# Performance work log

Measured on AMD Instinct MI355X. Metric: run time of the kernel, lower is better.

The kernel has to match this reference:

```python
import jax, jax.numpy as jnp
import numpy as np

HEADS = 4
TOKEN_DIM = 128
SCALE = (TOKEN_DIM // HEADS) ** -0.5


def _conv1x1(x, w, b):
    # x: (B,C,D,H,W), w: (O,C), b: (O,)
    return jnp.einsum('bcdhw,oc->bodhw', x, w) + b[None, :, None, None, None]


def _flatten(x):
    # (B,C,D,H,W) -> (B,L,C)
    B, C = x.shape[0], x.shape[1]
    return x.reshape(B, C, -1).transpose(0, 2, 1)


def _mha(q, k, v):
    # q: (B,Lq,D), k/v: (B,Lk,D)
    B, Lq, Dq = q.shape
    Lk = k.shape[1]
    hd = Dq // HEADS
    qh = q.reshape(B, Lq, HEADS, hd).transpose(0, 2, 1, 3)
    kh = k.reshape(B, Lk, HEADS, hd).transpose(0, 2, 1, 3)
    vh = v.reshape(B, Lk, HEADS, hd).transpose(0, 2, 1, 3)
    attn = jnp.einsum('bhqd,bhkd->bhqk', qh, kh) * SCALE
    attn = jax.nn.softmax(attn, axis=-1)
    out = jnp.einsum('bhqk,bhkd->bhqd', attn, vh)
    return out.transpose(0, 2, 1, 3).reshape(B, Lq, Dq)


def setup_inputs() -> dict:
    key = jax.random.key(0)
    ks = jax.random.split(key, 10)
    B, C, D, H, W = 2, 64, 16, 16, 16
    return {
        'feat_ct': jax.random.normal(ks[0], (B, C, D, H, W), jnp.float32),
        'feat_pet': jax.random.normal(ks[1], (B, C, D, H, W), jnp.float32),
        'wq': jax.random.normal(ks[2], (TOKEN_DIM, C), jnp.float32) * 0.05,
        'bq': jax.random.normal(ks[3], (TOKEN_DIM,), jnp.float32) * 0.05,
        'wk': jax.random.normal(ks[4], (TOKEN_DIM, C), jnp.float32) * 0.05,
        'bk': jax.random.normal(ks[5], (TOKEN_DIM,), jnp.float32) * 0.05,
        'wv': jax.random.normal(ks[6], (TOKEN_DIM, C), jnp.float32) * 0.05,
        'bv': jax.random.normal(ks[7], (TOKEN_DIM,), jnp.float32) * 0.05,
        'wo': jax.random.normal(ks[8], (C, TOKEN_DIM), jnp.float32) * 0.05,
        'bo': jax.random.normal(ks[9], (C,), jnp.float32) * 0.05,
    }


def reference(feat_ct, feat_pet, wq, bq, wk, bk, wv, bv, wo, bo):
    B, C, D, H, W = feat_ct.shape
    q_ct = _flatten(_conv1x1(feat_ct, wq, bq))
    k_ct = _flatten(_conv1x1(feat_ct, wk, bk))
    v_ct = _flatten(_conv1x1(feat_ct, wv, bv))
    q_pet = _flatten(_conv1x1(feat_pet, wq, bq))
    k_pet = _flatten(_conv1x1(feat_pet, wk, bk))
    v_pet = _flatten(_conv1x1(feat_pet, wv, bv))

    ct_attn = _mha(q_ct, k_pet, v_pet)
    pet_attn = _mha(q_pet, k_ct, v_ct)

    # Original torch code does view(B, token_dim, -1).permute(0,2,1) followed by
    # unflatten's permute(0,2,1) -> net effect is a raw reinterpretation of the
    # contiguous (B, L, token_dim) buffer as (B, token_dim, D, H, W): a reshape.
    fused_ct = ((ct_attn + q_ct) * 0.5).reshape(B, TOKEN_DIM, D, H, W)
    fused_ct = _conv1x1(fused_ct, wo, bo)  # dropout is identity (eval)
    fused_pet = ((pet_attn + q_pet) * 0.5).reshape(B, TOKEN_DIM, D, H, W)
    fused_pet = _conv1x1(fused_pet, wo, bo)

    return feat_ct + fused_ct, feat_pet + fused_pet
```

## Files before the change

### kernel.cpp

```cpp
#include <hip/hip_runtime.h>

typedef __bf16 bf16x8 __attribute__((ext_vector_type(8)));
typedef float f32x4 __attribute__((ext_vector_type(4)));
typedef float f32x16 __attribute__((ext_vector_type(16)));
typedef _Float16 f16x2 __attribute__((ext_vector_type(2)));
typedef unsigned short u16x8 __attribute__((ext_vector_type(8)));
typedef unsigned int u32x4 __attribute__((ext_vector_type(4)));
typedef unsigned int u32x2 __attribute__((ext_vector_type(2)));

constexpr int C_ = 64, TD_ = 128, L_ = 4096, B_ = 2, H_ = 4, HD_ = 32;
constexpr float SCALE_LOG2E = 0.25504821365f;

#if __has_builtin(__builtin_amdgcn_exp2f)
#define EXP2F __builtin_amdgcn_exp2f
#else
#define EXP2F exp2f
#endif

static __device__ __forceinline__ unsigned short f2bf(float f) {
  unsigned u = __builtin_bit_cast(unsigned, f);
  u += 0x7fffu + ((u >> 16) & 1u);
  return (unsigned short)(u >> 16);
}
static __device__ __forceinline__ float bf2f(unsigned short h) {
  unsigned u = ((unsigned)h) << 16;
  return __builtin_bit_cast(float, u);
}
static __device__ __forceinline__ unsigned cvt_pk_bf16(float lo, float hi) {
  unsigned r;
  asm("v_cvt_pk_bf16_f32 %0, %1, %2" : "=v"(r) : "v"(lo), "v"(hi));
  return r;
}
static __device__ __forceinline__ unsigned cvt_pk_f16(float lo, float hi) {
  return __builtin_bit_cast(unsigned, __builtin_amdgcn_cvt_pkrtz(lo, hi));
}
static __device__ __forceinline__ void plane_swap(unsigned& a, unsigned& b) {
  asm("v_permlane32_swap_b32 %0, %1" : "+v"(a), "+v"(b));
}
static __device__ __forceinline__ float xhalf_add(float x) {
  float a = x, b = x;
  asm("v_permlane32_swap_b32 %0, %1" : "+v"(a), "+v"(b));
  return a + b;
}
static __device__ __forceinline__ int rowf(int r, int hi) {
  return (r & 3) + 8 * (r >> 2) + 4 * hi;
}
static __device__ __forceinline__ bf16x8 pack8(const float* v) {
  unsigned p0 = cvt_pk_bf16(v[0], v[1]);
  unsigned p1 = cvt_pk_bf16(v[2], v[3]);
  unsigned p2 = cvt_pk_bf16(v[4], v[5]);
  unsigned p3 = cvt_pk_bf16(v[6], v[7]);
  return __builtin_bit_cast(bf16x8, (u32x4){p0, p1, p2, p3});
}

__global__ __launch_bounds__(256) void proj_kernel(
    const float* __restrict__ fct, const float* __restrict__ fpet,
    const float* __restrict__ wq, const float* __restrict__ bq,
    const float* __restrict__ wk, const float* __restrict__ bk,
    const float* __restrict__ wv, const float* __restrict__ bv,
    unsigned short* __restrict__ Qbf, unsigned short* __restrict__ Kbf,
    unsigned short* __restrict__ Vt, float* __restrict__ QT)
{
  __shared__ __align__(16) unsigned short Tb[32][136];

  int bid = blockIdx.x;
  int lt = bid & 127;
  int rest = bid >> 7;
  int mb = rest & 3;
  int which = rest >> 2;
  int l0 = lt * 32;
  int b = mb & 1;
  const float* xb = (mb >= 2 ? fpet : fct) + (size_t)b * C_ * L_;

  int lane = threadIdx.x & 63, wid = threadIdx.x >> 6;
  int l31 = lane & 31, hi = lane >> 5;
  int od = wid * 32;

  const float* W  = which == 0 ? wq : (which == 1 ? wk : wv);
  const float* Bs = which == 0 ? bq : (which == 1 ? bk : bv);

  const f32x16 Z = {0.f, 0.f, 0.f, 0.f, 0.f, 0.f, 0.f, 0.f,
                    0.f, 0.f, 0.f, 0.f, 0.f, 0.f, 0.f, 0.f};
  f32x16 acc = Z;
  #pragma unroll
  for (int ch = 0; ch < 4; ++ch) {
    float v[8], a[8];
    #pragma unroll
    for (int j = 0; j < 8; ++j)
      v[j] = xb[(size_t)(ch * 16 + hi * 8 + j) * L_ + l0 + l31];
    const float* wr = W + (size_t)(od + l31) * C_ + ch * 16 + hi * 8;
    #pragma unroll
    for (int j = 0; j < 8; ++j) a[j] = wr[j];
    acc = __builtin_amdgcn_mfma_f32_32x32x16_bf16(pack8(a), pack8(v), acc, 0, 0, 0);
  }

  if (which == 2) {
    #pragma unroll
    for (int r = 0; r < 16; ++r) {
      int o = od + rowf(r, hi);
      Vt[((size_t)mb * TD_ + o) * L_ + l0 + l31] = f2bf(acc[r] + Bs[o]);
    }
  } else {
    if (which == 0) {
      #pragma unroll
      for (int r = 0; r < 16; ++r) {
        int o = od + rowf(r, hi);
        QT[((size_t)mb * TD_ + o) * L_ + l0 + l31] = acc[r] + Bs[o];
      }
    }
    float sc = which == 0 ? SCALE_LOG2E : 1.0f;
    #pragma unroll
    for (int rg = 0; rg < 4; ++rg) {
      int cb = od + 8 * rg + 4 * hi;
      float y0 = (acc[rg * 4 + 0] + Bs[cb + 0]) * sc;
      float y1 = (acc[rg * 4 + 1] + Bs[cb + 1]) * sc;
      float y2 = (acc[rg * 4 + 2] + Bs[cb + 2]) * sc;
      float y3 = (acc[rg * 4 + 3] + Bs[cb + 3]) * sc;
      u32x2 pk = {cvt_pk_bf16(y0, y1), cvt_pk_bf16(y2, y3)};
      *(u32x2*)&Tb[l31][cb] = pk;
    }
    __syncthreads();
    unsigned short* dstg = which ? Kbf : Qbf;
    int row = threadIdx.x >> 3, chunk = threadIdx.x & 7;
    int h = chunk >> 1, d0 = (chunk & 1) * 16;
    u16x8 v0 = *(const u16x8*)&Tb[row][chunk * 16];
    u16x8 v1 = *(const u16x8*)&Tb[row][chunk * 16 + 8];
    size_t gb = (((size_t)mb * H_ + h) * L_ + l0 + row) * HD_ + d0;
    *(u16x8*)&dstg[gb] = v0;
    *(u16x8*)&dstg[gb + 8] = v1;
  }
}

static __device__ __forceinline__ void softmax_pv(
    const f32x16& S, float& lp, f32x16& O, bf16x8 vc0, bf16x8 vc1)
{
  float p[16];
  #pragma unroll
  for (int i = 0; i < 16; ++i) p[i] = EXP2F(S[i]);
  float s0 = (p[0] + p[1]) + (p[2] + p[3]);
  float s1 = (p[4] + p[5]) + (p[6] + p[7]);
  float s2 = (p[8] + p[9]) + (p[10] + p[11]);
  float s3 = (p[12] + p[13]) + (p[14] + p[15]);
  lp += (s0 + s1) + (s2 + s3);

  unsigned w0 = cvt_pk_bf16(p[0], p[1]);
  unsigned w1 = cvt_pk_bf16(p[2], p[3]);
  unsigned w2 = cvt_pk_bf16(p[4], p[5]);
  unsigned w3 = cvt_pk_bf16(p[6], p[7]);
  unsigned w4 = cvt_pk_bf16(p[8], p[9]);
  unsigned w5 = cvt_pk_bf16(p[10], p[11]);
  unsigned w6 = cvt_pk_bf16(p[12], p[13]);
  unsigned w7 = cvt_pk_bf16(p[14], p[15]);
  plane_swap(w0, w2);
  plane_swap(w1, w3);
  plane_swap(w4, w6);
  plane_swap(w5, w7);
  bf16x8 pf0 = __builtin_bit_cast(bf16x8, (u32x4){w0, w1, w2, w3});
  bf16x8 pf1 = __builtin_bit_cast(bf16x8, (u32x4){w4, w5, w6, w7});

  O = __builtin_amdgcn_mfma_f32_32x32x16_bf16(vc0, pf0, O, 0, 0, 0);
  O = __builtin_amdgcn_mfma_f32_32x32x16_bf16(vc1, pf1, O, 0, 0, 0);
}

__global__ __launch_bounds__(256, 4) void attn_kernel(
    const unsigned short* __restrict__ Qbf, const unsigned short* __restrict__ Kbf,
    const unsigned short* __restrict__ Vt, const float* __restrict__ QT,
    unsigned short* __restrict__ Fh, unsigned short* __restrict__ Fl)
{
  __shared__ __align__(16) unsigned Obuf[4][64][17];
  __shared__ float lbuf[4][64];

  int bid = blockIdx.x;
  int x = bid & 7, local = bid >> 3;
  int g = 2 * x + (local & 1);
  int qg = local >> 1;
  int h = g & 3, b = (g >> 2) & 1, dir = g >> 3;

  int lane = threadIdx.x & 63, wid = threadIdx.x >> 6;
  int l31 = lane & 31, hi = lane >> 5;
  int q0 = qg * 64;
  int qmb = dir * B_ + b, kmb = (1 - dir) * B_ + b;
  int k0 = wid * 1024;

  const unsigned short* qbase = Qbf + (size_t)(qmb * H_ + h) * L_ * HD_;
  bf16x8 qb[2][2];
  #pragma unroll
  for (int s = 0; s < 2; ++s)
    #pragma unroll
    for (int c = 0; c < 2; ++c)
      qb[s][c] = *(const bf16x8*)(qbase + (q0 + s * 32 + l31) * HD_ + c * 16 + hi * 8);

  const unsigned short* kp =
      Kbf + (size_t)(kmb * H_ + h) * L_ * HD_ + (k0 + l31) * HD_ + hi * 8;
  const unsigned short* vp =
      Vt + (size_t)(kmb * TD_ + h * HD_ + l31) * L_ + k0 + hi * 8;

  const f32x16 Z = {0.f, 0.f, 0.f, 0.f, 0.f, 0.f, 0.f, 0.f,
                    0.f, 0.f, 0.f, 0.f, 0.f, 0.f, 0.f, 0.f};
  f32x16 Oa[2] = {Z, Z};
  float lp[2] = {0.f, 0.f};

  bf16x8 kc0 = *(const bf16x8*)(kp);
  bf16x8 kc1 = *(const bf16x8*)(kp + 16);
  bf16x8 vc0 = *(const bf16x8*)(vp);
  bf16x8 vc1 = *(const bf16x8*)(vp + 16);

  #pragma unroll 4
  for (int t = 0; t < 32; ++t) {
    bf16x8 kn0 = *(const bf16x8*)(kp + (t + 1) * 1024);
    bf16x8 kn1 = *(const bf16x8*)(kp + (t + 1) * 1024 + 16);
    bf16x8 vn0 = *(const bf16x8*)(vp + (t + 1) * 32);
    bf16x8 vn1 = *(const bf16x8*)(vp + (t + 1) * 32 + 16);
    #pragma unroll
    for (int s = 0; s < 2; ++s) {
      f32x16 S = __builtin_amdgcn_mfma_f32_32x32x16_bf16(kc0, qb[s][0], Z, 0, 0, 0);
      S = __builtin_amdgcn_mfma_f32_32x32x16_bf16(kc1, qb[s][1], S, 0, 0, 0);
      softmax_pv(S, lp[s], Oa[s], vc0, vc1);
    }
    kc0 = kn0; kc1 = kn1; vc0 = vn0; vc1 = vn1;
  }

  lp[0] = xhalf_add(lp[0]);
  lp[1] = xhalf_add(lp[1]);
  if (hi == 0) {
    lbuf[wid][l31] = lp[0];
    lbuf[wid][32 + l31] = lp[1];
  }
  #pragma unroll
  for (int s = 0; s < 2; ++s)
    #pragma unroll
    for (int r = 0; r < 16; r += 2) {
      unsigned pk2 = cvt_pk_f16(Oa[s][r], Oa[s][r + 1]);
      int d2 = ((r & 3) >> 1) + 4 * (r >> 2) + 2 * hi;
      Obuf[wid][s * 32 + l31][d2] = pk2;
    }
  __syncthreads();

  float T = (lbuf[0][lane] + lbuf[1][lane]) + (lbuf[2][lane] + lbuf[3][lane]);
  float inv = 1.0f / T;
  const float* qtp = QT + ((size_t)qmb * TD_ + h * HD_) * L_ + q0 + lane;
  float vals[8];
  #pragma unroll
  for (int jp = 0; jp < 4; ++jp) {
    float se = 0.f, so = 0.f;
    #pragma unroll
    for (int w = 0; w < 4; ++w) {
      f16x2 v = __builtin_bit_cast(f16x2, Obuf[w][lane][wid * 4 + jp]);
      se += (float)v[0];
      so += (float)v[1];
    }
    int dd = wid * 8 + jp * 2;
    vals[jp * 2]     = (se * inv + qtp[(size_t)dd * L_]) * 0.5f;
    vals[jp * 2 + 1] = (so * inv + qtp[(size_t)(dd + 1) * L_]) * 0.5f;
  }
  __syncthreads();

  unsigned (*Sb)[64][17] = (unsigned (*)[64][17])Obuf;
  #pragma unroll
  for (int jp = 0; jp < 4; ++jp) {
    float v0 = vals[jp * 2], v1 = vals[jp * 2 + 1];
    float h0 = bf2f(f2bf(v0)), h1 = bf2f(f2bf(v1));
    Sb[0][lane][wid * 4 + jp] = cvt_pk_bf16(v0, v1);
    Sb[1][lane][wid * 4 + jp] = cvt_pk_bf16(v0 - h0, v1 - h1);
  }
  __syncthreads();
  int q = threadIdx.x >> 2, dq = threadIdx.x & 3;
  u32x4 vh = *(const u32x4*)&Sb[0][q][dq * 4];
  u32x4 vl = *(const u32x4*)&Sb[1][q][dq * 4];
  size_t gb = ((size_t)qmb * L_ + q0 + q) * TD_ + h * HD_ + dq * 8;
  *(u16x8*)&Fh[gb] = __builtin_bit_cast(u16x8, vh);
  *(u16x8*)&Fl[gb] = __builtin_bit_cast(u16x8, vl);
}

__global__ __launch_bounds__(256) void epi_kernel(
    const float* __restrict__ fct, const float* __restrict__ fpet,
    const float* __restrict__ wo, const float* __restrict__ bo,
    const unsigned short* __restrict__ Fh, const unsigned short* __restrict__ Fl,
    float* __restrict__ out)
{
  __shared__ __align__(16) unsigned short Gh[32][136], Gl[32][136];
  __shared__ __align__(16) float red[2][32][33];

  int bid = blockIdx.x;
  int lt = bid & 127, im = bid >> 7;
  int b = im & 1, d = im >> 1;
  int l0 = lt * 32;
  int lr = l0 >> 7, col0 = l0 & 127;

  int tid = threadIdx.x;
  int lane = tid & 63, wid = tid >> 6;
  int l31 = lane & 31, hi = lane >> 5;
  int mt = wid & 1, kh = wid >> 1;
  int c0 = mt * 32;

  bf16x8 Ah[4], Al[4];
  #pragma unroll
  for (int ch = 0; ch < 4; ++ch) {
    const float* wr = wo + (size_t)(c0 + l31) * TD_ + (kh * 4 + ch) * 16 + hi * 8;
    float ah[8], al[8];
    #pragma unroll
    for (int j = 0; j < 8; ++j) {
      float v = wr[j];
      float hf = bf2f(f2bf(v));
      ah[j] = hf;
      al[j] = v - hf;
    }
    Ah[ch] = pack8(ah);
    Al[ch] = pack8(al);
  }

  {
    int o = tid & 127, half = tid >> 7;
    size_t src = ((size_t)im * L_ + o * 32 + lr) * TD_ + col0 + half * 16;
    u16x8 ha = *(const u16x8*)&Fh[src];
    u16x8 hb = *(const u16x8*)&Fh[src + 8];
    u16x8 la = *(const u16x8*)&Fl[src];
    u16x8 lb = *(const u16x8*)&Fl[src + 8];
    #pragma unroll
    for (int j = 0; j < 8; ++j) {
      Gh[half * 16 + j][o] = ha[j];
      Gl[half * 16 + j][o] = la[j];
    }
    #pragma unroll
    for (int j = 0; j < 8; ++j) {
      Gh[half * 16 + 8 + j][o] = hb[j];
      Gl[half * 16 + 8 + j][o] = lb[j];
    }
  }
  __syncthreads();

  const f32x16 Z = {0.f, 0.f, 0.f, 0.f, 0.f, 0.f, 0.f, 0.f,
                    0.f, 0.f, 0.f, 0.f, 0.f, 0.f, 0.f, 0.f};
  f32x16 acc = Z;
  #pragma unroll
  for (int ch = 0; ch < 4; ++ch) {
    int ko = (kh * 4 + ch) * 16 + hi * 8;
    bf16x8 Bh = *(const bf16x8*)&Gh[l31][ko];
    bf16x8 Bl = *(const bf16x8*)&Gl[l31][ko];
    acc = __builtin_amdgcn_mfma_f32_32x32x16_bf16(Ah[ch], Bh, acc, 0, 0, 0);
    acc = __builtin_amdgcn_mfma_f32_32x32x16_bf16(Ah[ch], Bl, acc, 0, 0, 0);
    acc = __builtin_amdgcn_mfma_f32_32x32x16_bf16(Al[ch], Bh, acc, 0, 0, 0);
  }

  if (kh == 1) {
    #pragma unroll
    for (int r = 0; r < 16; ++r) red[mt][rowf(r, hi)][l31] = acc[r];
  }
  __syncthreads();
  if (kh == 0) {
    const float* feat = (d ? fpet : fct) + (size_t)b * C_ * L_;
    float* ob = out + (size_t)im * C_ * L_;
    int l = l0 + l31;
    #pragma unroll
    for (int r = 0; r < 16; ++r) {
      int row = rowf(r, hi);
      int c = c0 + row;
      float v = acc[r] + red[mt][row][l31];
      ob[(size_t)c * L_ + l] = feat[(size_t)c * L_ + l] + bo[c] + v;
    }
  }
}

extern "C" void kernel_launch(void* const* d_in, const int* in_sizes, int n_in,
                              void* d_out, int out_size, void* d_ws, size_t ws_size,
                              hipStream_t stream)
{
  const float* fct  = (const float*)d_in[0];
  const float* fpet = (const float*)d_in[1];
  const float* wq = (const float*)d_in[2];
  const float* bq = (const float*)d_in[3];
  const float* wk = (const float*)d_in[4];
  const float* bk = (const float*)d_in[5];
  const float* wv = (const float*)d_in[6];
  const float* bv = (const float*)d_in[7];
  const float* wo = (const float*)d_in[8];
  const float* bo = (const float*)d_in[9];
  float* out = (float*)d_out;

  unsigned short* Qbf = (unsigned short*)d_ws;
  unsigned short* Kbf = Qbf + 2097152;
  unsigned short* Vt  = Kbf + 2097152;
  float* QT = (float*)(Vt + 2097152);
  unsigned short* Fh = (unsigned short*)(QT + 2097152);
  unsigned short* Fl = Fh + 2097152;

  proj_kernel<<<1536, 256, 0, stream>>>(fct, fpet, wq, bq, wk, bk, wv, bv,
                                        Qbf, Kbf, Vt, QT);
  attn_kernel<<<1024, 256, 0, stream>>>(Qbf, Kbf, Vt, QT, Fh, Fl);
  epi_kernel<<<512, 256, 0, stream>>>(fct, fpet, wo, bo, Fh, Fl, out);
}
```

Baseline: 146.2 us.

## Stage projection inputs in LDS, pack softmax row sums, add MFMA priority hints

```diff
diff --git a/kernel.cpp b/kernel.cpp
--- a/kernel.cpp
+++ b/kernel.cpp
@@ -1,6 +1,7 @@
 #include <hip/hip_runtime.h>
 
 typedef __bf16 bf16x8 __attribute__((ext_vector_type(8)));
+typedef float f32x2 __attribute__((ext_vector_type(2)));
 typedef float f32x4 __attribute__((ext_vector_type(4)));
 typedef float f32x16 __attribute__((ext_vector_type(16)));
 typedef _Float16 f16x2 __attribute__((ext_vector_type(2)));
@@ -41,6 +42,11 @@
   float a = x, b = x;
   asm("v_permlane32_swap_b32 %0, %1" : "+v"(a), "+v"(b));
   return a + b;
+}
+static __device__ __forceinline__ f32x2 pk_add(f32x2 a, f32x2 b) {
+  f32x2 d;
+  asm("v_pk_add_f32 %0, %1, %2" : "=v"(d) : "v"(a), "v"(b));
+  return d;
 }
 static __device__ __forceinline__ int rowf(int r, int hi) {
   return (r & 3) + 8 * (r >> 2) + 4 * hi;
@@ -61,6 +67,7 @@
     unsigned short* __restrict__ Qbf, unsigned short* __restrict__ Kbf,
     unsigned short* __restrict__ Vt, float* __restrict__ QT)
 {
+  __shared__ __align__(16) float Xs[64][36];
   __shared__ __align__(16) unsigned short Tb[32][136];
 
   int bid = blockIdx.x;
@@ -72,9 +79,20 @@
   int b = mb & 1;
   const float* xb = (mb >= 2 ? fpet : fct) + (size_t)b * C_ * L_;
 
-  int lane = threadIdx.x & 63, wid = threadIdx.x >> 6;
+  int tid = threadIdx.x;
+  int lane = tid & 63, wid = tid >> 6;
   int l31 = lane & 31, hi = lane >> 5;
   int od = wid * 32;
+
+  {
+    int r = tid >> 2, c4 = tid & 3;
+    const float* s = xb + (size_t)r * L_ + l0 + c4 * 8;
+    f32x4 a0 = *(const f32x4*)(s);
+    f32x4 a1 = *(const f32x4*)(s + 4);
+    *(f32x4*)&Xs[r][c4 * 8] = a0;
+    *(f32x4*)&Xs[r][c4 * 8 + 4] = a1;
+  }
+  __syncthreads();
 
   const float* W  = which == 0 ? wq : (which == 1 ? wk : wv);
   const float* Bs = which == 0 ? bq : (which == 1 ? bk : bv);
@@ -87,7 +105,7 @@
     float v[8], a[8];
     #pragma unroll
     for (int j = 0; j < 8; ++j)
-      v[j] = xb[(size_t)(ch * 16 + hi * 8 + j) * L_ + l0 + l31];
+      v[j] = Xs[ch * 16 + hi * 8 + j][l31];
     const float* wr = W + (size_t)(od + l31) * C_ + ch * 16 + hi * 8;
     #pragma unroll
     for (int j = 0; j < 8; ++j) a[j] = wr[j];
@@ -121,7 +139,7 @@
     }
     __syncthreads();
     unsigned short* dstg = which ? Kbf : Qbf;
-    int row = threadIdx.x >> 3, chunk = threadIdx.x & 7;
+    int row = tid >> 3, chunk = tid & 7;
     int h = chunk >> 1, d0 = (chunk & 1) * 16;
     u16x8 v0 = *(const u16x8*)&Tb[row][chunk * 16];
     u16x8 v1 = *(const u16x8*)&Tb[row][chunk * 16 + 8];
@@ -132,16 +150,20 @@
 }
 
 static __device__ __forceinline__ void softmax_pv(
-    const f32x16& S, float& lp, f32x16& O, bf16x8 vc0, bf16x8 vc1)
+    const f32x16& S, f32x2& lp2, f32x16& O, bf16x8 vc0, bf16x8 vc1)
 {
   float p[16];
   #pragma unroll
   for (int i = 0; i < 16; ++i) p[i] = EXP2F(S[i]);
-  float s0 = (p[0] + p[1]) + (p[2] + p[3]);
-  float s1 = (p[4] + p[5]) + (p[6] + p[7]);
-  float s2 = (p[8] + p[9]) + (p[10] + p[11]);
-  float s3 = (p[12] + p[13]) + (p[14] + p[15]);
-  lp += (s0 + s1) + (s2 + s3);
+
+  f32x2 q0 = pk_add((f32x2){p[0], p[1]}, (f32x2){p[2], p[3]});
+  f32x2 q1 = pk_add((f32x2){p[4], p[5]}, (f32x2){p[6], p[7]});
+  f32x2 q2 = pk_add((f32x2){p[8], p[9]}, (f32x2){p[10], p[11]});
+  f32x2 q3 = pk_add((f32x2){p[12], p[13]}, (f32x2){p[14], p[15]});
+  q0 = pk_add(q0, q1);
+  q2 = pk_add(q2, q3);
+  q0 = pk_add(q0, q2);
+  lp2 = pk_add(lp2, q0);
 
   unsigned w0 = cvt_pk_bf16(p[0], p[1]);
   unsigned w1 = cvt_pk_bf16(p[2], p[3]);
@@ -158,8 +180,10 @@
   bf16x8 pf0 = __builtin_bit_cast(bf16x8, (u32x4){w0, w1, w2, w3});
   bf16x8 pf1 = __builtin_bit_cast(bf16x8, (u32x4){w4, w5, w6, w7});
 
+  __builtin_amdgcn_s_setprio(1);
   O = __builtin_amdgcn_mfma_f32_32x32x16_bf16(vc0, pf0, O, 0, 0, 0);
   O = __builtin_amdgcn_mfma_f32_32x32x16_bf16(vc1, pf1, O, 0, 0, 0);
+  __builtin_amdgcn_s_setprio(0);
 }
 
 __global__ __launch_bounds__(256, 4) void attn_kernel(
@@ -198,7 +222,7 @@
   const f32x16 Z = {0.f, 0.f, 0.f, 0.f, 0.f, 0.f, 0.f, 0.f,
                     0.f, 0.f, 0.f, 0.f, 0.f, 0.f, 0.f, 0.f};
   f32x16 Oa[2] = {Z, Z};
-  float lp[2] = {0.f, 0.f};
+  f32x2 lp2[2] = {(f32x2){0.f, 0.f}, (f32x2){0.f, 0.f}};
 
   bf16x8 kc0 = *(const bf16x8*)(kp);
   bf16x8 kc1 = *(const bf16x8*)(kp + 16);
@@ -213,18 +237,20 @@
     bf16x8 vn1 = *(const bf16x8*)(vp + (t + 1) * 32 + 16);
     #pragma unroll
     for (int s = 0; s < 2; ++s) {
+      __builtin_amdgcn_s_setprio(1);
       f32x16 S = __builtin_amdgcn_mfma_f32_32x32x16_bf16(kc0, qb[s][0], Z, 0, 0, 0);
       S = __builtin_amdgcn_mfma_f32_32x32x16_bf16(kc1, qb[s][1], S, 0, 0, 0);
-      softmax_pv(S, lp[s], Oa[s], vc0, vc1);
+      __builtin_amdgcn_s_setprio(0);
+      softmax_pv(S, lp2[s], Oa[s], vc0, vc1);
     }
     kc0 = kn0; kc1 = kn1; vc0 = vn0; vc1 = vn1;
   }
 
-  lp[0] = xhalf_add(lp[0]);
-  lp[1] = xhalf_add(lp[1]);
+  float lpa = xhalf_add(lp2[0][0] + lp2[0][1]);
+  float lpb = xhalf_add(lp2[1][0] + lp2[1][1]);
   if (hi == 0) {
-    lbuf[wid][l31] = lp[0];
-    lbuf[wid][32 + l31] = lp[1];
+    lbuf[wid][l31] = lpa;
+    lbuf[wid][32 + l31] = lpb;
   }
   #pragma unroll
   for (int s = 0; s < 2; ++s)
@@ -236,16 +262,17 @@
     }
   __syncthreads();
 
-  float T = (lbuf[0][lane] + lbuf[1][lane]) + (lbuf[2][lane] + lbuf[3][lane]);
+  int lane_ = threadIdx.x & 63;
+  float T = (lbuf[0][lane_] + lbuf[1][lane_]) + (lbuf[2][lane_] + lbuf[3][lane_]);
   float inv = 1.0f / T;
-  const float* qtp = QT + ((size_t)qmb * TD_ + h * HD_) * L_ + q0 + lane;
+  const float* qtp = QT + ((size_t)qmb * TD_ + h * HD_) * L_ + q0 + lane_;
   float vals[8];
   #pragma unroll
   for (int jp = 0; jp < 4; ++jp) {
     float se = 0.f, so = 0.f;
     #pragma unroll
     for (int w = 0; w < 4; ++w) {
-      f16x2 v = __builtin_bit_cast(f16x2, Obuf[w][lane][wid * 4 + jp]);
+      f16x2 v = __builtin_bit_cast(f16x2, Obuf[w][lane_][wid * 4 + jp]);
       se += (float)v[0];
       so += (float)v[1];
     }
@@ -260,8 +287,8 @@
   for (int jp = 0; jp < 4; ++jp) {
     float v0 = vals[jp * 2], v1 = vals[jp * 2 + 1];
     float h0 = bf2f(f2bf(v0)), h1 = bf2f(f2bf(v1));
-    Sb[0][lane][wid * 4 + jp] = cvt_pk_bf16(v0, v1);
-    Sb[1][lane][wid * 4 + jp] = cvt_pk_bf16(v0 - h0, v1 - h1);
+    Sb[0][lane_][wid * 4 + jp] = cvt_pk_bf16(v0, v1);
+    Sb[1][lane_][wid * 4 + jp] = cvt_pk_bf16(v0 - h0, v1 - h1);
   }
   __syncthreads();
   int q = threadIdx.x >> 2, dq = threadIdx.x & 3;
```

Result: faster. 142.1 us (-2.8%).
